# Kernel tuning notes

Measured on AMD Instinct MI355X. Metric: run time of the kernel, lower is better.

## Reference

```python
import jax, jax.numpy as jnp
import numpy as np

N = 50000
E = 400000
IN_DIM = 256
HID = 64
HEADS = 8
OUT_DIM = 40
NEG_SLOPE = 0.2  # PyG GATConv leaky-relu slope


def gat_conv(x, src, dst, W, a_src, a_dst, bias, concat):
    """One PyG-style GATConv (eval mode, self-loops already appended).
    x: [N, in], W: [in, H*C], a_src/a_dst: [H, C], bias: [H*C] or [C]."""
    H, C = a_src.shape
    h = (x @ W).reshape(N, H, C)                       # [N, H, C]
    # per-node attention logits, gathered per edge
    e_src = (h * a_src[None]).sum(-1)                  # [N, H]
    e_dst = (h * a_dst[None]).sum(-1)                  # [N, H]
    alpha = jax.nn.leaky_relu(e_src[src] + e_dst[dst], NEG_SLOPE)  # [Etot, H]
    # segment softmax over incoming edges of each dst node
    amax = jax.ops.segment_max(alpha, dst, num_segments=N)         # [N, H]
    ex = jnp.exp(alpha - amax[dst])
    denom = jax.ops.segment_sum(ex, dst, num_segments=N)           # [N, H]
    coef = ex / denom[dst]                                         # [Etot, H]
    # weighted scatter-add of neighbor features
    msg = h[src] * coef[:, :, None]                                # [Etot, H, C]
    out = jax.ops.segment_sum(msg, dst, num_segments=N)            # [N, H, C]
    out = out.reshape(N, H * C) if concat else out.mean(axis=1)
    return out + bias


def setup_inputs() -> dict:
    key = jax.random.key(0)
    ks = jax.random.split(key, 10)
    x = jax.random.normal(ks[0], (N, IN_DIM), dtype=jnp.float32)
    edge_index = jax.random.randint(ks[1], (2, E), 0, N, dtype=jnp.int32)
    g1 = 1.0 / np.sqrt(IN_DIM)
    g2 = 1.0 / np.sqrt(HID * HEADS)
    W1 = jax.random.normal(ks[2], (IN_DIM, HEADS * HID), dtype=jnp.float32) * g1
    a_src1 = jax.random.normal(ks[3], (HEADS, HID), dtype=jnp.float32) * 0.1
    a_dst1 = jax.random.normal(ks[4], (HEADS, HID), dtype=jnp.float32) * 0.1
    b1 = jnp.zeros((HEADS * HID,), dtype=jnp.float32)
    W2 = jax.random.normal(ks[5], (HEADS * HID, OUT_DIM), dtype=jnp.float32) * g2
    a_src2 = jax.random.normal(ks[6], (1, OUT_DIM), dtype=jnp.float32) * 0.1
    a_dst2 = jax.random.normal(ks[7], (1, OUT_DIM), dtype=jnp.float32) * 0.1
    b2 = jnp.zeros((OUT_DIM,), dtype=jnp.float32)
    return {"x": x, "edge_index": edge_index, "W1": W1, "a_src1": a_src1,
            "a_dst1": a_dst1, "b1": b1, "W2": W2, "a_src2": a_src2,
            "a_dst2": a_dst2, "b2": b2}


def reference(x, edge_index, W1, a_src1, a_dst1, b1, W2, a_src2, a_dst2, b2):
    # append self loops (PyG GATConv default add_self_loops=True)
    loop = jnp.arange(N, dtype=edge_index.dtype)
    src = jnp.concatenate([edge_index[0], loop])
    dst = jnp.concatenate([edge_index[1], loop])
    h = gat_conv(x, src, dst, W1, a_src1, a_dst1, b1, concat=True)
    h = jax.nn.elu(h)
    # dropout is identity in eval mode
    out = gat_conv(h, src, dst, W2, a_src2, a_dst2, b2, concat=False)
    return out
```

## Files before the change

kernel.cpp:

```cpp
#include <hip/hip_runtime.h>
#include <hip/hip_bf16.h>
#include <math.h>

#define IN_DIM 256
#define HEADS 8
#define HID 64
#define HC1 512
#define OUT_DIM 40
#define NEG_SLOPE 0.2f

typedef __attribute__((ext_vector_type(8))) short short8;
typedef __attribute__((ext_vector_type(4))) float f32x4;

__device__ __forceinline__ unsigned short f2b(float f) {
    __hip_bfloat16 h = __float2bfloat16(f);
    unsigned short u;
    __builtin_memcpy(&u, &h, 2);
    return u;
}

#define LRELU(a) ((a) > 0.f ? (a) : NEG_SLOPE * (a))

#define NB_W ((HC1 * IN_DIM + 48 * HC1 + 255) / 256)

__global__ __launch_bounds__(256) void prologue_kernel(
    const float* __restrict__ W1, const float* __restrict__ W2,
    __hip_bfloat16* __restrict__ W1T, __hip_bfloat16* __restrict__ W2T,
    const int* __restrict__ ei, int* __restrict__ deg, int E, int ET)
{
    int b = blockIdx.x;
    if (b < NB_W) {
        int i = b * 256 + threadIdx.x;
        if (i < HC1 * IN_DIM) {
            int n = i >> 8, k = i & 255;
            W1T[i] = __float2bfloat16(W1[(size_t)k * HC1 + n]);
        }
        int j = i - HC1 * IN_DIM;
        if (j >= 0 && j < 48 * HC1) {
            int n = j >> 9, k = j & 511;
            W2T[j] = __float2bfloat16(n < OUT_DIM ? W2[(size_t)k * OUT_DIM + n] : 0.f);
        }
    } else {
        int e = (b - NB_W) * 256 + threadIdx.x;
        if (e >= ET) return;
        int d = (e < E) ? ei[E + e] : e - E;
        atomicAdd(&deg[d], 1);
    }
}


__global__ __launch_bounds__(256) void scan1_kernel(
    const int* __restrict__ deg, int* __restrict__ rowptr,
    int* __restrict__ aux, int N)
{
    __shared__ int sd[256];
    int tid = threadIdx.x;
    int i = blockIdx.x * 256 + tid;
    int v = (i < N) ? deg[i] : 0;
    sd[tid] = v;
    __syncthreads();
    for (int off = 1; off < 256; off <<= 1) {
        int t = (tid >= off) ? sd[tid - off] : 0;
        __syncthreads();
        sd[tid] += t;
        __syncthreads();
    }
    if (i < N) rowptr[i] = sd[tid] - v;
    if (tid == 255) aux[blockIdx.x] = sd[255];
}

__global__ __launch_bounds__(256) void scan_finish_kernel(
    int* __restrict__ rowptr, int* __restrict__ cursor,
    const int* __restrict__ aux, int N, int ET)
{
    __shared__ int sd[256];
    int tid = threadIdx.x;
    sd[tid] = (tid < blockIdx.x) ? aux[tid] : 0;
    __syncthreads();
#pragma unroll
    for (int off = 128; off > 0; off >>= 1) {
        if (tid < off) sd[tid] += sd[tid + off];
        __syncthreads();
    }
    int prefix = sd[0];
    int i = blockIdx.x * 256 + tid;
    if (i < N) {
        int v = rowptr[i] + prefix;
        rowptr[i] = v;
        cursor[i] = v;
    }
    if (i == 0) rowptr[N] = ET;
}

__global__ __launch_bounds__(256) void build_kernel(
    const int* __restrict__ ei, int* __restrict__ cursor,
    int* __restrict__ csr_src, int E, int ET)
{
    int e = blockIdx.x * 256 + threadIdx.x;
    if (e >= ET) return;
    int s, d;
    if (e < E) { s = ei[e]; d = ei[E + e]; } else { s = d = e - E; }
    int pos = atomicAdd(&cursor[d], 1);
    csr_src[pos] = s;
}

__global__ __launch_bounds__(512) void gemm1_mfma(
    const float* __restrict__ x, const __hip_bfloat16* __restrict__ W1T,
    const float* __restrict__ a_src1, const float* __restrict__ a_dst1,
    __hip_bfloat16* __restrict__ h1, float* __restrict__ e_src1,
    float* __restrict__ e_dst1, int N)
{
    __shared__ __hip_bfloat16 As[64][264];
    const int tid = threadIdx.x;
    const int row0 = blockIdx.x * 64;
    const int w = tid >> 6;
    const int lane = tid & 63;
    const int r = lane & 15, g = lane >> 4;

    const short* bp = (const short*)W1T + (size_t)(w * 64 + r) * IN_DIM + 8 * g;
    short8 breg[8][4];
#pragma unroll
    for (int k8 = 0; k8 < 8; ++k8)
#pragma unroll
        for (int t = 0; t < 4; ++t)
            breg[k8][t] = *(const short8*)(bp + (size_t)t * 16 * IN_DIM + k8 * 32);

    {
        int rr = tid >> 3;
        int cb = (tid & 7) * 32;
        int rowc = row0 + rr; if (rowc >= N) rowc = N - 1;
        const float* xp = x + (size_t)rowc * IN_DIM + cb;
#pragma unroll
        for (int j = 0; j < 4; ++j) {
            float4 a0 = *(const float4*)(xp + 8 * j);
            float4 a1 = *(const float4*)(xp + 8 * j + 4);
            short8 v;
            v[0] = f2b(a0.x); v[1] = f2b(a0.y); v[2] = f2b(a0.z); v[3] = f2b(a0.w);
            v[4] = f2b(a1.x); v[5] = f2b(a1.y); v[6] = f2b(a1.z); v[7] = f2b(a1.w);
            *(short8*)(&As[rr][cb + 8 * j]) = v;
        }
    }
    __syncthreads();

    f32x4 acc[4][4] = {};
#pragma unroll
    for (int k8 = 0; k8 < 8; ++k8) {
        short8 af[4];
#pragma unroll
        for (int rt = 0; rt < 4; ++rt)
            af[rt] = *(const short8*)(&As[rt * 16 + r][k8 * 32 + 8 * g]);
#pragma unroll
        for (int t = 0; t < 4; ++t)
#pragma unroll
            for (int rt = 0; rt < 4; ++rt)
                acc[rt][t] = __builtin_amdgcn_mfma_f32_16x16x32_bf16(
                    af[rt], breg[k8][t], acc[rt][t], 0, 0, 0);
    }

#pragma unroll
    for (int rt = 0; rt < 4; ++rt)
#pragma unroll
        for (int t = 0; t < 4; ++t) {
            int c = w * 64 + t * 16 + r;
#pragma unroll
            for (int q = 0; q < 4; ++q) {
                int row = row0 + rt * 16 + 4 * g + q;
                if (row < N)
                    h1[(size_t)row * HC1 + c] = __float2bfloat16(acc[rt][t][q]);
            }
        }

    float a1v[4], a2v[4];
#pragma unroll
    for (int t = 0; t < 4; ++t) {
        a1v[t] = a_src1[w * 64 + t * 16 + r];
        a2v[t] = a_dst1[w * 64 + t * 16 + r];
    }
#pragma unroll
    for (int rt = 0; rt < 4; ++rt) {
        float ps[4] = {}, pd[4] = {};
#pragma unroll
        for (int t = 0; t < 4; ++t)
#pragma unroll
            for (int q = 0; q < 4; ++q) {
                ps[q] += acc[rt][t][q] * a1v[t];
                pd[q] += acc[rt][t][q] * a2v[t];
            }
#pragma unroll
        for (int off = 1; off < 16; off <<= 1)
#pragma unroll
            for (int q = 0; q < 4; ++q) {
                ps[q] += __shfl_xor(ps[q], off);
                pd[q] += __shfl_xor(pd[q], off);
            }
        if (r == 0) {
#pragma unroll
            for (int q = 0; q < 4; ++q) {
                int row = row0 + rt * 16 + 4 * g + q;
                if (row < N) {
                    e_src1[row * 8 + w] = ps[q];
                    e_dst1[row * 8 + w] = pd[q];
                }
            }
        }
    }
}

__global__ __launch_bounds__(256) void gather1_kernel(
    const int* __restrict__ rowptr, const int* __restrict__ csr_src,
    const __hip_bfloat16* __restrict__ h1, const float* __restrict__ e_src,
    const float* __restrict__ e_dst, const float* __restrict__ b1,
    __hip_bfloat16* __restrict__ hmid, int N)
{
    int d = blockIdx.x * 4 + (threadIdx.x >> 6);
    if (d >= N) return;
    const int lane = threadIdx.x & 63;
    const int h0 = lane >> 3;
    const int base = rowptr[d];
    const int deg = rowptr[d + 1] - base;
    const float edv = e_dst[d * 8 + (lane & 7)];

    float acc[8] = {};
    float ssum = 0.f;

    const int nch = (deg + 7) >> 3;
    for (int c = 0; c < nch; ++c) {
        int i = c * 8 + (lane >> 3);
        int ii = i < deg ? i : deg - 1;
        int s = csr_src[base + ii];
        float v = e_src[s * 8 + (lane & 7)] + edv;
        float coef = (i < deg) ? __expf(LRELU(v)) : 0.f;

        int emax = deg - c * 8; if (emax > 8) emax = 8;
        for (int e = 0; e < emax; ++e) {
            float ce = __shfl(coef, e * 8 + h0);
            int se = __shfl(s, e * 8);
            uint4 u = *(const uint4*)(h1 + ((size_t)se << 9) + 8 * lane);
            acc[0] += ce * __uint_as_float(u.x << 16);
            acc[1] += ce * __uint_as_float(u.x & 0xffff0000u);
            acc[2] += ce * __uint_as_float(u.y << 16);
            acc[3] += ce * __uint_as_float(u.y & 0xffff0000u);
            acc[4] += ce * __uint_as_float(u.z << 16);
            acc[5] += ce * __uint_as_float(u.z & 0xffff0000u);
            acc[6] += ce * __uint_as_float(u.w << 16);
            acc[7] += ce * __uint_as_float(u.w & 0xffff0000u);
            ssum += ce;
        }
    }

    float inv = 1.f / ssum;
    float4 b0 = *(const float4*)(b1 + 8 * lane);
    float4 b4 = *(const float4*)(b1 + 8 * lane + 4);
    float ob[8];
    ob[0] = acc[0] * inv + b0.x; ob[1] = acc[1] * inv + b0.y;
    ob[2] = acc[2] * inv + b0.z; ob[3] = acc[3] * inv + b0.w;
    ob[4] = acc[4] * inv + b4.x; ob[5] = acc[5] * inv + b4.y;
    ob[6] = acc[6] * inv + b4.z; ob[7] = acc[7] * inv + b4.w;
    unsigned short rr[8];
#pragma unroll
    for (int j = 0; j < 8; ++j) {
        float o = ob[j];
        o = o > 0.f ? o : expm1f(o);
        rr[j] = f2b(o);
    }
    *(uint4*)(hmid + (size_t)d * HC1 + 8 * lane) = *(uint4*)rr;
}

__global__ __launch_bounds__(256) void gemm2_mfma(
    const __hip_bfloat16* __restrict__ hmid, const __hip_bfloat16* __restrict__ W2T,
    const float* __restrict__ a_src2, const float* __restrict__ a_dst2,
    float* __restrict__ h2, float* __restrict__ e_src2, float* __restrict__ e_dst2,
    int N)
{
    __shared__ __hip_bfloat16 Bs[48][520];
    const int tid = threadIdx.x;
    const int w = tid >> 6;
    const int lane = tid & 63;
    const int r = lane & 15, g = lane >> 4;
    const int rowW = blockIdx.x * 64 + w * 16;

    int arow = rowW + r; if (arow >= N) arow = N - 1;
    const short* ap = (const short*)hmid + (size_t)arow * HC1 + 8 * g;
    short8 areg[16];
#pragma unroll
    for (int kk = 0; kk < 16; ++kk)
        areg[kk] = *(const short8*)(ap + kk * 32);

    {
        const short* wp = (const short*)W2T;
#pragma unroll
        for (int i = 0; i < 12; ++i) {
            int idx = tid + i * 256;
            int row = idx >> 6, ch = idx & 63;
            *(short8*)(&Bs[row][ch * 8]) = *(const short8*)(wp + (size_t)row * HC1 + ch * 8);
        }
    }
    __syncthreads();

    f32x4 acc[3] = {};
#pragma unroll
    for (int kk = 0; kk < 16; ++kk) {
        short8 bf[3];
#pragma unroll
        for (int t = 0; t < 3; ++t)
            bf[t] = *(const short8*)(&Bs[t * 16 + r][kk * 32 + 8 * g]);
#pragma unroll
        for (int t = 0; t < 3; ++t)
            acc[t] = __builtin_amdgcn_mfma_f32_16x16x32_bf16(areg[kk], bf[t], acc[t], 0, 0, 0);
    }

#pragma unroll
    for (int t = 0; t < 3; ++t) {
        int c = t * 16 + r;
        if (c < OUT_DIM) {
#pragma unroll
            for (int q = 0; q < 4; ++q) {
                int row = rowW + 4 * g + q;
                if (row < N) h2[(size_t)row * OUT_DIM + c] = acc[t][q];
            }
        }
    }

    float as[3], ad[3];
#pragma unroll
    for (int t = 0; t < 3; ++t) {
        int c = t * 16 + r;
        as[t] = (c < OUT_DIM) ? a_src2[c] : 0.f;
        ad[t] = (c < OUT_DIM) ? a_dst2[c] : 0.f;
    }
    float ps[4] = {}, pd[4] = {};
#pragma unroll
    for (int t = 0; t < 3; ++t)
#pragma unroll
        for (int q = 0; q < 4; ++q) {
            ps[q] += acc[t][q] * as[t];
            pd[q] += acc[t][q] * ad[t];
        }
#pragma unroll
    for (int off = 1; off < 16; off <<= 1)
#pragma unroll
        for (int q = 0; q < 4; ++q) {
            ps[q] += __shfl_xor(ps[q], off);
            pd[q] += __shfl_xor(pd[q], off);
        }
    if (r == 0) {
#pragma unroll
        for (int q = 0; q < 4; ++q) {
            int row = rowW + 4 * g + q;
            if (row < N) { e_src2[row] = ps[q]; e_dst2[row] = pd[q]; }
        }
    }
}

__global__ __launch_bounds__(256) void gather2_kernel(
    const int* __restrict__ rowptr, const int* __restrict__ csr_src,
    const float* __restrict__ h2, const float* __restrict__ e_src,
    const float* __restrict__ e_dst, const float* __restrict__ b2,
    float* __restrict__ out, int N)
{
    int wid = (blockIdx.x * blockDim.x + threadIdx.x) >> 6;
    if (wid >= N) return;
    int lane = threadIdx.x & 63;
    int base = rowptr[wid], end = rowptr[wid + 1];
    float ed = e_dst[wid];
    bool act = lane < OUT_DIM;
    int ln = act ? lane : 0;

    float acc = 0.f, ssum = 0.f;
    int j = base;
    for (; j + 4 <= end; j += 4) {
        int s0 = csr_src[j], s1 = csr_src[j + 1], s2 = csr_src[j + 2], s3 = csr_src[j + 3];
        float v0 = e_src[s0] + ed, v1 = e_src[s1] + ed;
        float v2 = e_src[s2] + ed, v3 = e_src[s3] + ed;
        float f0 = h2[(size_t)s0 * OUT_DIM + ln];
        float f1 = h2[(size_t)s1 * OUT_DIM + ln];
        float f2 = h2[(size_t)s2 * OUT_DIM + ln];
        float f3 = h2[(size_t)s3 * OUT_DIM + ln];
        float e0 = __expf(LRELU(v0)), e1 = __expf(LRELU(v1));
        float e2 = __expf(LRELU(v2)), e3 = __expf(LRELU(v3));
        acc += e0 * f0 + e1 * f1 + e2 * f2 + e3 * f3;
        ssum += e0 + e1 + e2 + e3;
    }
    for (; j < end; ++j) {
        int s0 = csr_src[j];
        float v0 = e_src[s0] + ed;
        float f0 = h2[(size_t)s0 * OUT_DIM + ln];
        float e0 = __expf(LRELU(v0));
        acc += e0 * f0;
        ssum += e0;
    }
    if (act)
        out[(size_t)wid * OUT_DIM + lane] = acc / ssum + b2[lane];
}

extern "C" void kernel_launch(void* const* d_in, const int* in_sizes, int n_in,
                              void* d_out, int out_size, void* d_ws, size_t ws_size,
                              hipStream_t stream)
{
    const float* x      = (const float*)d_in[0];
    const int*   ei     = (const int*)d_in[1];
    const float* W1     = (const float*)d_in[2];
    const float* a_src1 = (const float*)d_in[3];
    const float* a_dst1 = (const float*)d_in[4];
    const float* b1     = (const float*)d_in[5];
    const float* W2     = (const float*)d_in[6];
    const float* a_src2 = (const float*)d_in[7];
    const float* a_dst2 = (const float*)d_in[8];
    const float* b2     = (const float*)d_in[9];
    float* out = (float*)d_out;

    const int N  = in_sizes[0] / IN_DIM;
    const int E  = in_sizes[1] / 2;
    const int ET = E + N;

    char* p = (char*)d_ws;
    auto alloc = [&](size_t bytes) -> void* {
        void* r = (void*)p;
        p += (bytes + 255) & ~(size_t)255;
        return r;
    };
    __hip_bfloat16* h1b    = (__hip_bfloat16*)alloc((size_t)N * HC1 * 2);
    __hip_bfloat16* hmid   = (__hip_bfloat16*)alloc((size_t)N * HC1 * 2);
    float*    h2      = (float*)alloc((size_t)N * OUT_DIM * 4);
    float*    e_src1  = (float*)alloc((size_t)N * HEADS * 4);
    float*    e_dst1  = (float*)alloc((size_t)N * HEADS * 4);
    float*    e_src2  = (float*)alloc((size_t)N * 4);
    float*    e_dst2  = (float*)alloc((size_t)N * 4);
    int*      deg     = (int*)alloc((size_t)N * 4);
    int*      rowptr  = (int*)alloc((size_t)(N + 1) * 4);
    int*      cursor  = (int*)alloc((size_t)N * 4);
    int*      csr_src = (int*)alloc((size_t)ET * 4);
    int*      aux     = (int*)alloc(256 * 4);
    __hip_bfloat16* W1T = (__hip_bfloat16*)alloc((size_t)HC1 * IN_DIM * 2);
    __hip_bfloat16* W2T = (__hip_bfloat16*)alloc((size_t)48 * HC1 * 2);

    const int nbN  = (N + 255) / 256;
    const int nbET = (ET + 255) / 256;

    hipMemsetAsync(deg, 0, (size_t)N * 4, stream);
    prologue_kernel<<<NB_W + nbET, 256, 0, stream>>>(W1, W2, W1T, W2T, ei, deg, E, ET);

    scan1_kernel<<<nbN, 256, 0, stream>>>(deg, rowptr, aux, N);
    scan_finish_kernel<<<nbN, 256, 0, stream>>>(rowptr, cursor, aux, N, ET);
    build_kernel<<<nbET, 256, 0, stream>>>(ei, cursor, csr_src, E, ET);

    gemm1_mfma<<<(N + 63) / 64, 512, 0, stream>>>(x, W1T, a_src1, a_dst1, h1b,
                                                  e_src1, e_dst1, N);
    gather1_kernel<<<(N + 3) / 4, 256, 0, stream>>>(rowptr, csr_src, h1b, e_src1,
                                                    e_dst1, b1, hmid, N);

    gemm2_mfma<<<(N + 63) / 64, 256, 0, stream>>>(hmid, W2T, a_src2, a_dst2, h2,
                                                  e_src2, e_dst2, N);
    gather2_kernel<<<(N + 3) / 4, 256, 0, stream>>>(rowptr, csr_src, h2, e_src2,
                                                    e_dst2, b2, out, N);
}
```

Measured before the change: 238.9 us.

## Fuse CSR build into GEMM1 launch, stream B operands, store h2 as bf16

Merges the CSR build kernel into the first GEMM launch: extra blocks at the front do the atomic scatter while the remaining blocks run the GEMM. That removes one launch and lets the two independent pieces of work overlap. GEMM1 now loads W1T fragments from global memory inside the K loop instead of preloading them all into registers, and GEMM2 streams its A fragments the same way. Both changes are meant to reduce register pressure and raise occupancy, at the cost of more load latency inside the loop. h2 is stored as bf16 to halve the gather2 traffic, which adds some rounding error.

```diff
diff --git a/kernel.cpp b/kernel.cpp
--- a/kernel.cpp
+++ b/kernel.cpp
@@ -92,38 +92,28 @@
     if (i == 0) rowptr[N] = ET;
 }
 
-__global__ __launch_bounds__(256) void build_kernel(
-    const int* __restrict__ ei, int* __restrict__ cursor,
-    int* __restrict__ csr_src, int E, int ET)
-{
-    int e = blockIdx.x * 256 + threadIdx.x;
-    if (e >= ET) return;
-    int s, d;
-    if (e < E) { s = ei[e]; d = ei[E + e]; } else { s = d = e - E; }
-    int pos = atomicAdd(&cursor[d], 1);
-    csr_src[pos] = s;
-}
-
-__global__ __launch_bounds__(512) void gemm1_mfma(
+__global__ __launch_bounds__(512) void gemm1_build(
     const float* __restrict__ x, const __hip_bfloat16* __restrict__ W1T,
     const float* __restrict__ a_src1, const float* __restrict__ a_dst1,
     __hip_bfloat16* __restrict__ h1, float* __restrict__ e_src1,
-    float* __restrict__ e_dst1, int N)
-{
+    float* __restrict__ e_dst1,
+    const int* __restrict__ ei, int* __restrict__ cursor,
+    int* __restrict__ csr_src, int buildBlocks, int E, int ET, int N)
+{
+    if ((int)blockIdx.x < buildBlocks) {
+        int e = blockIdx.x * 512 + threadIdx.x;
+        if (e < ET) {
+            int s, d;
+            if (e < E) { s = ei[e]; d = ei[E + e]; } else { s = d = e - E; }
+            int pos = atomicAdd(&cursor[d], 1);
+            csr_src[pos] = s;
+        }
+        return;
+    }
+
     __shared__ __hip_bfloat16 As[64][264];
     const int tid = threadIdx.x;
-    const int row0 = blockIdx.x * 64;
-    const int w = tid >> 6;
-    const int lane = tid & 63;
-    const int r = lane & 15, g = lane >> 4;
-
-    const short* bp = (const short*)W1T + (size_t)(w * 64 + r) * IN_DIM + 8 * g;
-    short8 breg[8][4];
-#pragma unroll
-    for (int k8 = 0; k8 < 8; ++k8)
-#pragma unroll
-        for (int t = 0; t < 4; ++t)
-            breg[k8][t] = *(const short8*)(bp + (size_t)t * 16 * IN_DIM + k8 * 32);
+    const int row0 = (blockIdx.x - buildBlocks) * 64;
 
     {
         int rr = tid >> 3;
@@ -142,19 +132,29 @@
     }
     __syncthreads();
 
+    const int w = tid >> 6;
+    const int lane = tid & 63;
+    const int r = lane & 15, g = lane >> 4;
+
     f32x4 acc[4][4] = {};
-#pragma unroll
-    for (int k8 = 0; k8 < 8; ++k8) {
+    const short* bp = (const short*)W1T + (size_t)(w * 64 + r) * IN_DIM + 8 * g;
+
+#pragma unroll 2
+    for (int kk = 0; kk < IN_DIM; kk += 32) {
         short8 af[4];
 #pragma unroll
         for (int rt = 0; rt < 4; ++rt)
-            af[rt] = *(const short8*)(&As[rt * 16 + r][k8 * 32 + 8 * g]);
+            af[rt] = *(const short8*)(&As[rt * 16 + r][kk + 8 * g]);
+        short8 bf[4];
+#pragma unroll
+        for (int t = 0; t < 4; ++t)
+            bf[t] = *(const short8*)(bp + (size_t)t * 16 * IN_DIM + kk);
 #pragma unroll
         for (int t = 0; t < 4; ++t)
 #pragma unroll
             for (int rt = 0; rt < 4; ++rt)
                 acc[rt][t] = __builtin_amdgcn_mfma_f32_16x16x32_bf16(
-                    af[rt], breg[k8][t], acc[rt][t], 0, 0, 0);
+                    af[rt], bf[t], acc[rt][t], 0, 0, 0);
     }
 
 #pragma unroll
@@ -269,11 +269,23 @@
 __global__ __launch_bounds__(256) void gemm2_mfma(
     const __hip_bfloat16* __restrict__ hmid, const __hip_bfloat16* __restrict__ W2T,
     const float* __restrict__ a_src2, const float* __restrict__ a_dst2,
-    float* __restrict__ h2, float* __restrict__ e_src2, float* __restrict__ e_dst2,
-    int N)
+    __hip_bfloat16* __restrict__ h2, float* __restrict__ e_src2,
+    float* __restrict__ e_dst2, int N)
 {
     __shared__ __hip_bfloat16 Bs[48][520];
     const int tid = threadIdx.x;
+
+    {
+        const short* wp = (const short*)W2T;
+#pragma unroll
+        for (int i = 0; i < 12; ++i) {
+            int idx = tid + i * 256;
+            int row = idx >> 6, ch = idx & 63;
+            *(short8*)(&Bs[row][ch * 8]) = *(const short8*)(wp + (size_t)row * HC1 + ch * 8);
+        }
+    }
+    __syncthreads();
+
     const int w = tid >> 6;
     const int lane = tid & 63;
     const int r = lane & 15, g = lane >> 4;
@@ -281,32 +293,18 @@
 
     int arow = rowW + r; if (arow >= N) arow = N - 1;
     const short* ap = (const short*)hmid + (size_t)arow * HC1 + 8 * g;
-    short8 areg[16];
-#pragma unroll
-    for (int kk = 0; kk < 16; ++kk)
-        areg[kk] = *(const short8*)(ap + kk * 32);
-
-    {
-        const short* wp = (const short*)W2T;
-#pragma unroll
-        for (int i = 0; i < 12; ++i) {
-            int idx = tid + i * 256;
-            int row = idx >> 6, ch = idx & 63;
-            *(short8*)(&Bs[row][ch * 8]) = *(const short8*)(wp + (size_t)row * HC1 + ch * 8);
-        }
-    }
-    __syncthreads();
 
     f32x4 acc[3] = {};
-#pragma unroll
-    for (int kk = 0; kk < 16; ++kk) {
+#pragma unroll 4
+    for (int kk = 0; kk < HC1; kk += 32) {
+        short8 af = *(const short8*)(ap + kk);
         short8 bf[3];
 #pragma unroll
         for (int t = 0; t < 3; ++t)
-            bf[t] = *(const short8*)(&Bs[t * 16 + r][kk * 32 + 8 * g]);
+            bf[t] = *(const short8*)(&Bs[t * 16 + r][kk + 8 * g]);
 #pragma unroll
         for (int t = 0; t < 3; ++t)
-            acc[t] = __builtin_amdgcn_mfma_f32_16x16x32_bf16(areg[kk], bf[t], acc[t], 0, 0, 0);
+            acc[t] = __builtin_amdgcn_mfma_f32_16x16x32_bf16(af, bf[t], acc[t], 0, 0, 0);
     }
 
 #pragma unroll
@@ -316,7 +314,7 @@
 #pragma unroll
             for (int q = 0; q < 4; ++q) {
                 int row = rowW + 4 * g + q;
-                if (row < N) h2[(size_t)row * OUT_DIM + c] = acc[t][q];
+                if (row < N) h2[(size_t)row * OUT_DIM + c] = __float2bfloat16(acc[t][q]);
             }
         }
     }
@@ -354,7 +352,7 @@
 
 __global__ __launch_bounds__(256) void gather2_kernel(
     const int* __restrict__ rowptr, const int* __restrict__ csr_src,
-    const float* __restrict__ h2, const float* __restrict__ e_src,
+    const __hip_bfloat16* __restrict__ h2, const float* __restrict__ e_src,
     const float* __restrict__ e_dst, const float* __restrict__ b2,
     float* __restrict__ out, int N)
 {
@@ -365,6 +363,7 @@
     float ed = e_dst[wid];
     bool act = lane < OUT_DIM;
     int ln = act ? lane : 0;
+    const unsigned short* h2u = (const unsigned short*)h2;
 
     float acc = 0.f, ssum = 0.f;
     int j = base;
@@ -372,21 +371,22 @@
         int s0 = csr_src[j], s1 = csr_src[j + 1], s2 = csr_src[j + 2], s3 = csr_src[j + 3];
         float v0 = e_src[s0] + ed, v1 = e_src[s1] + ed;
         float v2 = e_src[s2] + ed, v3 = e_src[s3] + ed;
-        float f0 = h2[(size_t)s0 * OUT_DIM + ln];
-        float f1 = h2[(size_t)s1 * OUT_DIM + ln];
-        float f2 = h2[(size_t)s2 * OUT_DIM + ln];
-        float f3 = h2[(size_t)s3 * OUT_DIM + ln];
+        unsigned f0 = h2u[(size_t)s0 * OUT_DIM + ln];
+        unsigned f1 = h2u[(size_t)s1 * OUT_DIM + ln];
+        unsigned f2 = h2u[(size_t)s2 * OUT_DIM + ln];
+        unsigned f3 = h2u[(size_t)s3 * OUT_DIM + ln];
         float e0 = __expf(LRELU(v0)), e1 = __expf(LRELU(v1));
         float e2 = __expf(LRELU(v2)), e3 = __expf(LRELU(v3));
-        acc += e0 * f0 + e1 * f1 + e2 * f2 + e3 * f3;
+        acc += e0 * __uint_as_float(f0 << 16) + e1 * __uint_as_float(f1 << 16)
+             + e2 * __uint_as_float(f2 << 16) + e3 * __uint_as_float(f3 << 16);
         ssum += e0 + e1 + e2 + e3;
     }
     for (; j < end; ++j) {
         int s0 = csr_src[j];
         float v0 = e_src[s0] + ed;
-        float f0 = h2[(size_t)s0 * OUT_DIM + ln];
+        unsigned f0 = h2u[(size_t)s0 * OUT_DIM + ln];
         float e0 = __expf(LRELU(v0));
-        acc += e0 * f0;
+        acc += e0 * __uint_as_float(f0 << 16);
         ssum += e0;
     }
     if (act)
@@ -421,7 +421,7 @@
     };
     __hip_bfloat16* h1b    = (__hip_bfloat16*)alloc((size_t)N * HC1 * 2);
     __hip_bfloat16* hmid   = (__hip_bfloat16*)alloc((size_t)N * HC1 * 2);
-    float*    h2      = (float*)alloc((size_t)N * OUT_DIM * 4);
+    __hip_bfloat16* h2     = (__hip_bfloat16*)alloc((size_t)N * OUT_DIM * 2);
     float*    e_src1  = (float*)alloc((size_t)N * HEADS * 4);
     float*    e_dst1  = (float*)alloc((size_t)N * HEADS * 4);
     float*    e_src2  = (float*)alloc((size_t)N * 4);
@@ -434,18 +434,20 @@
     __hip_bfloat16* W1T = (__hip_bfloat16*)alloc((size_t)HC1 * IN_DIM * 2);
     __hip_bfloat16* W2T = (__hip_bfloat16*)alloc((size_t)48 * HC1 * 2);
 
-    const int nbN  = (N + 255) / 256;
-    const int nbET = (ET + 255) / 256;
+    const int nbN    = (N + 255) / 256;
+    const int nbET   = (ET + 255) / 256;
+    const int nbB512 = (ET + 511) / 512;
+    const int nbG    = (N + 63) / 64;
 
     hipMemsetAsync(deg, 0, (size_t)N * 4, stream);
     prologue_kernel<<<NB_W + nbET, 256, 0, stream>>>(W1, W2, W1T, W2T, ei, deg, E, ET);
 
     scan1_kernel<<<nbN, 256, 0, stream>>>(deg, rowptr, aux, N);
     scan_finish_kernel<<<nbN, 256, 0, stream>>>(rowptr, cursor, aux, N, ET);
-    build_kernel<<<nbET, 256, 0, stream>>>(ei, cursor, csr_src, E, ET);
-
-    gemm1_mfma<<<(N + 63) / 64, 512, 0, stream>>>(x, W1T, a_src1, a_dst1, h1b,
-                                                  e_src1, e_dst1, N);
+
+    gemm1_build<<<nbB512 + nbG, 512, 0, stream>>>(x, W1T, a_src1, a_dst1, h1b,
+                                                  e_src1, e_dst1, ei, cursor,
+                                                  csr_src, nbB512, E, ET, N);
     gather1_kernel<<<(N + 3) / 4, 256, 0, stream>>>(rowptr, csr_src, h1b, e_src1,
                                                     e_dst1, b1, hmid, N);
 
```

Measured after the change: 222.9 us. 6.7% less time.
